# Performance work log

Hardware: AMD Instinct MI355X
Metric: run time of the kernel (lower is better)

## Reference

```python
import jax, jax.numpy as jnp
import numpy as np

B, D, H, F, L, M, MEM, ACT, STO, HID = 2048, 1024, 8, 4096, 2, 256, 16, 32, 1024, 1024
HD = D // H
SCALE = HD ** -0.5
EPS = 1e-4


def rmsnorm(x, w):
    return x * jax.lax.rsqrt(jnp.mean(x * x, axis=-1, keepdims=True) + EPS) * w


def setup_inputs() -> dict:
    key = jax.random.key(0)
    ks = iter(jax.random.split(key, 32))

    def nrm(shape, scale=0.02):
        return jax.random.normal(next(ks), shape, dtype=jnp.float32) * scale

    return {
        'stoch': jax.random.normal(next(ks), (B, STO), dtype=jnp.float32),
        'deter': jax.random.normal(next(ks), (B, D), dtype=jnp.float32),
        'action': jax.random.normal(next(ks), (B, ACT), dtype=jnp.float32),
        'memory': jax.random.normal(next(ks), (B, MEM, D), dtype=jnp.float32),
        'inp_w1': nrm((STO + ACT, HID)), 'inp_b1': jnp.zeros((HID,), jnp.float32),
        'inp_nw': jnp.ones((HID,), jnp.float32),
        'inp_w2': nrm((HID, D)), 'inp_b2': jnp.zeros((D,), jnp.float32),
        'Wq': nrm((L, D, D)), 'bq': jnp.zeros((L, D), jnp.float32),
        'Wk': nrm((L, D, D)), 'bk': jnp.zeros((L, D), jnp.float32),
        'Wv': nrm((L, D, D)), 'bv': jnp.zeros((L, D), jnp.float32),
        'Wo': nrm((L, D, D)), 'bo': jnp.zeros((L, D), jnp.float32),
        'rel_emb': nrm((L, 2 * M + 1, H)),
        'n1w': jnp.ones((L, D), jnp.float32), 'n2w': jnp.ones((L, D), jnp.float32),
        'ffw1': nrm((L, D, F)), 'ffb1': jnp.zeros((L, F), jnp.float32),
        'ffw2': nrm((L, F, D)), 'ffb2': jnp.zeros((L, D), jnp.float32),
        'fnw': jnp.ones((D,), jnp.float32),
    }


def reference(stoch, deter, action, memory, inp_w1, inp_b1, inp_nw, inp_w2, inp_b2,
              Wq, bq, Wk, bk, Wv, bv, Wo, bo, rel_emb, n1w, n2w,
              ffw1, ffb1, ffw2, ffb2, fnw):
    # action normalization: denominator is detached in torch
    a = action / jax.lax.stop_gradient(jnp.maximum(jnp.abs(action), 1.0))
    tok = jnp.concatenate([stoch.reshape(stoch.shape[0], -1), a], axis=-1)
    tok = jax.nn.silu(rmsnorm(tok @ inp_w1 + inp_b1, inp_nw)) @ inp_w2 + inp_b2  # [B,D]
    seq = jnp.concatenate([memory, tok[:, None, :]], axis=1)  # [B,S,D], S = MEM+1
    S = seq.shape[1]
    rel = jnp.clip(jnp.arange(S)[:, None] - jnp.arange(S)[None, :], -M, M) + M  # [S,S]
    for l in range(L):
        xn = rmsnorm(seq, n1w[l])
        q = (xn @ Wq[l] + bq[l]).reshape(-1, S, H, HD)
        k = (xn @ Wk[l] + bk[l]).reshape(-1, S, H, HD)
        v = (xn @ Wv[l] + bv[l]).reshape(-1, S, H, HD)
        bias = rel_emb[l][rel].transpose(2, 0, 1)  # [H,S,S]
        scores = jnp.einsum('bqhd,bkhd->bhqk', q, k) * SCALE + bias[None]
        probs = jax.nn.softmax(scores, axis=-1)
        att = jnp.einsum('bhqk,bkhd->bqhd', probs, v).reshape(-1, S, D)
        seq = seq + (att @ Wo[l] + bo[l])
        xn2 = rmsnorm(seq, n2w[l])
        seq = seq + (jax.nn.gelu(xn2 @ ffw1[l] + ffb1[l], approximate=False) @ ffw2[l] + ffb2[l])
    new_deter = rmsnorm(seq[:, -1] + deter, fnw)
    new_mem = jax.lax.stop_gradient(seq[:, -MEM:])
    return (new_deter, new_mem)
```

## Files before the change

### kernel.cpp

```cpp
#include <hip/hip_runtime.h>
#include <hip/hip_bf16.h>
#include <math.h>

#define NB 2048
#define ND 1024
#define NH 8
#define NHD 128
#define NF 4096
#define NL 2
#define NMEM 16
#define NS 17
#define NROWS (NB*NS)
#define NTOK 1056
#define SCALE_ATT 0.08838834764831845f

typedef unsigned short u16;
typedef unsigned int u32;

typedef __bf16 bf16x8 __attribute__((ext_vector_type(8)));
typedef float f32x4 __attribute__((ext_vector_type(4)));

__device__ __forceinline__ float bf2f(u16 h) {
  union { u32 u; float f; } c; c.u = ((u32)h) << 16; return c.f;
}
__device__ __forceinline__ u16 f2bf(float f) {
  union { float ff; u32 u; } c; c.ff = f;
  return (u16)((c.u + 0x7FFFu + ((c.u >> 16) & 1u)) >> 16);
}
__device__ __forceinline__ bf16x8 as_b8(uint4 u) {
  union { uint4 u; bf16x8 b; } c; c.u = u; return c.b;
}

__device__ __forceinline__ void gload16(const void* g, void* l) {
  __builtin_amdgcn_global_load_lds(
      (const __attribute__((address_space(1))) void*)(uintptr_t)g,
      (__attribute__((address_space(3))) void*)(u32)(uintptr_t)l,
      16, 0, 0);
}

__device__ __forceinline__ float gelu_fast(float x) {
  float u = x * (0.7978845608f + 0.0356774081f * x * x);
  return x * (1.0f / (1.0f + __expf(-2.0f * u)));
}

__device__ __forceinline__ void pack_tile(const float* __restrict__ src,
                                          u16* __restrict__ dst,
                                          int K, int N, int n0, int k0,
                                          float* tile )
{
  int tx = threadIdx.x & 31, ty = threadIdx.x >> 5;
#pragma unroll
  for (int r = ty; r < 32; r += 8)
    tile[r * 33 + tx] = src[(size_t)(k0 + r) * N + n0 + tx];
  __syncthreads();
#pragma unroll
  for (int r = ty; r < 32; r += 8)
    dst[(size_t)(n0 + r) * K + k0 + tx] = f2bf(tile[tx * 33 + r]);
}

__global__ __launch_bounds__(256)
void pack_wT_k(const float* __restrict__ src, u16* __restrict__ dst, int K, int N)
{
  __shared__ float tile[32 * 33];
  pack_tile(src, dst, K, N, blockIdx.x * 32, blockIdx.y * 32, tile);
}

__global__ __launch_bounds__(256)
void pack_layer_k(const float* __restrict__ wq, const float* __restrict__ wk,
                  const float* __restrict__ wv, const float* __restrict__ wo,
                  const float* __restrict__ w1, const float* __restrict__ w2,
                  const float* __restrict__ bq, const float* __restrict__ bk,
                  const float* __restrict__ bv,
                  u16* __restrict__ qkvT, u16* __restrict__ oT,
                  u16* __restrict__ f1T, u16* __restrict__ f2T,
                  float* __restrict__ BQKV)
{
  __shared__ float tile[32 * 33];
  int id = blockIdx.x;
  if (id < 4096) {
    int which = id >> 10, l = id & 1023;
    const float* src = which == 0 ? wq : which == 1 ? wk : which == 2 ? wv : wo;
    u16* dst = which == 3 ? oT : qkvT + (size_t)which * 1048576;
    pack_tile(src, dst, 1024, 1024, (l & 31) * 32, (l >> 5) * 32, tile);
  } else if (id < 8192) {
    int l = id - 4096;
    pack_tile(w1, f1T, 1024, 4096, (l & 127) * 32, (l >> 7) * 32, tile);
  } else if (id < 12288) {
    int l = id - 8192;
    pack_tile(w2, f2T, 4096, 1024, (l & 31) * 32, (l >> 5) * 32, tile);
  } else {
    int j = (id - 12288) * 256 + threadIdx.x;
    if (j < 3072)
      BQKV[j] = (j < 1024) ? bq[j] : (j < 2048 ? bk[j - 1024] : bv[j - 2048]);
  }
}

template<int EPI>
__global__ __launch_bounds__(256)
void gemm2_k(const u16* __restrict__ A, int lda,
             const u16* __restrict__ BT, int ldb,
             const float* __restrict__ bias,
             u16* __restrict__ Cb, int ldc,
             int K)
{
  __shared__ __align__(16) u16 Asm[2][128 * 32];
  __shared__ __align__(16) u16 Bsm[2][128 * 32];
  const int tid  = threadIdx.x;
  const int lane = tid & 63;
  const int wv   = tid >> 6;
  const int wm   = wv >> 1, wn = wv & 1;
  const int lr   = lane & 15;
  const int kb   = lane >> 4;

  const int gx = gridDim.x;
  const int nwg = gx * gridDim.y;
  int bid = blockIdx.y * gx + blockIdx.x;
  if ((nwg & 7) == 0) bid = (bid & 7) * (nwg >> 3) + (bid >> 3);
  const int bx = bid % gx, by = bid / gx;
  const long bmBase = (long)by * 128;
  const int  bnBase = bx * 128;

  const int srow = tid >> 2;
  const int skc  = ((tid & 3) ^ ((srow >> 1) & 3)) * 8;
  const u16* aG0 = A  + (size_t)(bmBase + srow) * lda + skc;
  const u16* aG1 = aG0 + (size_t)64 * lda;
  const u16* bG0 = BT + (size_t)(bnBase + srow) * ldb + skc;
  const u16* bG1 = bG0 + (size_t)64 * ldb;
  const int wbase = (tid & ~63) * 8;
  const int rslot = (kb ^ ((lr >> 1) & 3)) * 8;

  f32x4 acc[4][4];
#pragma unroll
  for (int m = 0; m < 4; ++m)
#pragma unroll
    for (int n = 0; n < 4; ++n)
      acc[m][n] = (f32x4){0.0f, 0.0f, 0.0f, 0.0f};

  const int nk = K >> 5;
  {
    u16* aL = &Asm[0][wbase];
    u16* bL = &Bsm[0][wbase];
    gload16(aG0, aL);
    gload16(aG1, aL + 2048);
    gload16(bG0, bL);
    gload16(bG1, bL + 2048);
  }
  asm volatile("s_waitcnt vmcnt(0)" ::: "memory");
  __builtin_amdgcn_s_barrier();

  for (int i = 0; i < nk; ++i) {
    const int cur = i & 1;
    if (i + 1 < nk) {
      const int kt = (i + 1) << 5;
      u16* aL = &Asm[cur ^ 1][wbase];
      u16* bL = &Bsm[cur ^ 1][wbase];
      gload16(aG0 + kt, aL);
      gload16(aG1 + kt, aL + 2048);
      gload16(bG0 + kt, bL);
      gload16(bG1 + kt, bL + 2048);
    }
    bf16x8 af[4], bfv[4];
#pragma unroll
    for (int m = 0; m < 4; ++m)
      af[m] = as_b8(*(const uint4*)&Asm[cur][(wm * 64 + m * 16 + lr) * 32 + rslot]);
#pragma unroll
    for (int n = 0; n < 4; ++n)
      bfv[n] = as_b8(*(const uint4*)&Bsm[cur][(wn * 64 + n * 16 + lr) * 32 + rslot]);
#pragma unroll
    for (int m = 0; m < 4; ++m)
#pragma unroll
      for (int n = 0; n < 4; ++n)
        acc[m][n] = __builtin_amdgcn_mfma_f32_16x16x32_bf16(af[m], bfv[n], acc[m][n], 0, 0, 0);
    asm volatile("s_waitcnt vmcnt(0)" ::: "memory");
    __builtin_amdgcn_s_barrier();
  }

#pragma unroll
  for (int m = 0; m < 4; ++m) {
#pragma unroll
    for (int n = 0; n < 4; ++n) {
      int gcol = bnBase + wn * 64 + n * 16 + lr;
      float bv = bias[gcol];
      long growb = bmBase + wm * 64 + m * 16 + (lane >> 4) * 4;
#pragma unroll
      for (int i = 0; i < 4; ++i) {
        float val = acc[m][n][i] + bv;
        long row = growb + i;
        u16* p = Cb + (size_t)row * ldc + gcol;
        if (EPI == 1) val = gelu_fast(val);
        if (EPI == 2) val += bf2f(*p);
        *p = f2bf(val);
      }
    }
  }
}

__global__ __launch_bounds__(256)
void prep_tokcat_k(const float* __restrict__ stoch, const float* __restrict__ action,
                   u16* __restrict__ tok)
{
  size_t idx = (size_t)blockIdx.x * 256 + threadIdx.x;
  if (idx >= (size_t)NB * NTOK) return;
  int b = (int)(idx / NTOK), j = (int)(idx % NTOK);
  float v;
  if (j < 1024) {
    v = stoch[(size_t)b * 1024 + j];
  } else {
    float a = action[(size_t)b * 32 + (j - 1024)];
    v = a / fmaxf(fabsf(a), 1.0f);
  }
  tok[idx] = f2bf(v);
}

__global__ __launch_bounds__(256)
void rmsnorm_bf16_k(const u16* __restrict__ X, const float* __restrict__ w,
                    u16* __restrict__ Y)
{
  const int wv = threadIdx.x >> 6, lane = threadIdx.x & 63;
  const size_t row = (size_t)blockIdx.x * 4 + wv;
  const u16* x = X + row * 1024 + lane * 16;
  union { u16 s[16]; uint4 u[2]; } iv;
  iv.u[0] = ((const uint4*)x)[0];
  iv.u[1] = ((const uint4*)x)[1];
  float f[16];
  float ss = 0.0f;
#pragma unroll
  for (int j = 0; j < 16; ++j) { f[j] = bf2f(iv.s[j]); ss += f[j] * f[j]; }
#pragma unroll
  for (int o = 1; o < 64; o <<= 1) ss += __shfl_xor(ss, o, 64);
  const float r = rsqrtf(ss * (1.0f / 1024.0f) + 1e-4f);
  const float* wp = w + lane * 16;
  union { u16 s[16]; uint4 u[2]; } ob;
#pragma unroll
  for (int j = 0; j < 16; ++j) ob.s[j] = f2bf(f[j] * r * wp[j]);
  uint4* dst = (uint4*)(Y + row * 1024 + lane * 16);
  dst[0] = ob.u[0];
  dst[1] = ob.u[1];
}

__global__ __launch_bounds__(256)
void rmsnorm_silu_k(u16* __restrict__ X, const float* __restrict__ w)
{
  const int wv = threadIdx.x >> 6, lane = threadIdx.x & 63;
  const size_t row = (size_t)blockIdx.x * 4 + wv;
  u16* x = X + row * 1024 + lane * 16;
  union { u16 s[16]; uint4 u[2]; } iv;
  iv.u[0] = ((const uint4*)x)[0];
  iv.u[1] = ((const uint4*)x)[1];
  float f[16];
  float ss = 0.0f;
#pragma unroll
  for (int j = 0; j < 16; ++j) { f[j] = bf2f(iv.s[j]); ss += f[j] * f[j]; }
#pragma unroll
  for (int o = 1; o < 64; o <<= 1) ss += __shfl_xor(ss, o, 64);
  const float r = rsqrtf(ss * (1.0f / 1024.0f) + 1e-4f);
  const float* wp = w + lane * 16;
  union { u16 s[16]; uint4 u[2]; } ob;
#pragma unroll
  for (int j = 0; j < 16; ++j) {
    float n = f[j] * r * wp[j];
    ob.s[j] = f2bf(n / (1.0f + __expf(-n)));
  }
  ((uint4*)x)[0] = ob.u[0];
  ((uint4*)x)[1] = ob.u[1];
}

__global__ __launch_bounds__(256)
void init_seq_k(const float* __restrict__ mem, u16* __restrict__ seq)
{
  size_t idx = ((size_t)blockIdx.x * 256 + threadIdx.x) * 8;
  if (idx >= (size_t)NB * 16 * 1024) return;
  size_t b = idx / (16 * 1024), rem = idx % (16 * 1024);
  float4 v0 = *(const float4*)&mem[idx];
  float4 v1 = *(const float4*)&mem[idx + 4];
  union { u16 s[8]; uint4 u; } ob;
  ob.s[0] = f2bf(v0.x); ob.s[1] = f2bf(v0.y); ob.s[2] = f2bf(v0.z); ob.s[3] = f2bf(v0.w);
  ob.s[4] = f2bf(v1.x); ob.s[5] = f2bf(v1.y); ob.s[6] = f2bf(v1.z); ob.s[7] = f2bf(v1.w);
  *(uint4*)&seq[b * (size_t)NS * 1024 + rem] = ob.u;
}

__global__ __launch_bounds__(256)
void copy_mem_k(const u16* __restrict__ seq, float* __restrict__ out)
{
  size_t idx = ((size_t)blockIdx.x * 256 + threadIdx.x) * 8;
  if (idx >= (size_t)NB * 16 * 1024) return;
  size_t b = idx / (16 * 1024), rem = idx % (16 * 1024);
  union { u16 s[8]; uint4 u; } iv;
  iv.u = *(const uint4*)&seq[b * (size_t)NS * 1024 + 1024 + rem];
  float4 o0, o1;
  o0.x = bf2f(iv.s[0]); o0.y = bf2f(iv.s[1]); o0.z = bf2f(iv.s[2]); o0.w = bf2f(iv.s[3]);
  o1.x = bf2f(iv.s[4]); o1.y = bf2f(iv.s[5]); o1.z = bf2f(iv.s[6]); o1.w = bf2f(iv.s[7]);
  *(float4*)&out[idx] = o0;
  *(float4*)&out[idx + 4] = o1;
}

__global__ __launch_bounds__(256)
void final_deter_k(const u16* __restrict__ seq, const float* __restrict__ deter,
                   const float* __restrict__ fnw, float* __restrict__ out)
{
  int b = blockIdx.x;
  const u16* xs = seq + ((size_t)b * NS + 16) * 1024;
  const float* dt = deter + (size_t)b * 1024;
  int t = threadIdx.x;
  union { u16 s[4]; uint2 u; } iv;
  iv.u = *(const uint2*)&xs[t * 4];
  float v[4];
#pragma unroll
  for (int j = 0; j < 4; ++j) v[j] = bf2f(iv.s[j]) + dt[t * 4 + j];
  float ss = v[0] * v[0] + v[1] * v[1] + v[2] * v[2] + v[3] * v[3];
#pragma unroll
  for (int o = 1; o < 64; o <<= 1) ss += __shfl_xor(ss, o, 64);
  __shared__ float red[4];
  if ((t & 63) == 0) red[t >> 6] = ss;
  __syncthreads();
  float tot = red[0] + red[1] + red[2] + red[3];
  float r = rsqrtf(tot * (1.0f / 1024.0f) + 1e-4f);
  float4 ov;
  ov.x = v[0] * r * fnw[t * 4 + 0];
  ov.y = v[1] * r * fnw[t * 4 + 1];
  ov.z = v[2] * r * fnw[t * 4 + 2];
  ov.w = v[3] * r * fnw[t * 4 + 3];
  *(float4*)&out[(size_t)b * 1024 + t * 4] = ov;
}

#define LSTR 132
__global__ __launch_bounds__(256)
void attn_k(const u16* __restrict__ QKV, const float* __restrict__ rel,
            u16* __restrict__ O)
{
  __shared__ float qs[NS * LSTR];
  __shared__ float ks[NS * LSTR];
  __shared__ float vs[NS * LSTR];
  __shared__ float sc[NS * 20];
  int bh = blockIdx.x;
  int b = bh >> 3, h = bh & 7;
  int t = threadIdx.x;
  const size_t rowb = (size_t)b * NS * 3072 + h * 128;
  for (int e = t; e < NS * 16; e += 256) {
    int i = e >> 4, d = (e & 15) * 8;
    size_t off = rowb + (size_t)i * 3072 + d;
    uint4 q4 = *(const uint4*)(QKV + off);
    uint4 k4 = *(const uint4*)(QKV + off + 1024);
    uint4 v4 = *(const uint4*)(QKV + off + 2048);
    const u16* qp = (const u16*)&q4;
    const u16* kp = (const u16*)&k4;
    const u16* vp = (const u16*)&v4;
#pragma unroll
    for (int j = 0; j < 8; ++j) {
      qs[i * LSTR + d + j] = bf2f(qp[j]);
      ks[i * LSTR + d + j] = bf2f(kp[j]);
      vs[i * LSTR + d + j] = bf2f(vp[j]);
    }
  }
  __syncthreads();
  for (int e = t; e < NS * NS; e += 256) {
    int i = e / NS, j = e % NS;
    const float4* q4 = (const float4*)&qs[i * LSTR];
    const float4* k4 = (const float4*)&ks[j * LSTR];
    float s = 0.0f;
#pragma unroll
    for (int dd = 0; dd < 32; ++dd) {
      float4 a = q4[dd], bb = k4[dd];
      s += a.x * bb.x + a.y * bb.y + a.z * bb.z + a.w * bb.w;
    }
    sc[i * 20 + j] = s * SCALE_ATT + rel[(i - j + 256) * 8 + h];
  }
  __syncthreads();
  if (t < NS) {
    float mx = -1e30f;
    for (int j = 0; j < NS; ++j) mx = fmaxf(mx, sc[t * 20 + j]);
    float sum = 0.0f;
    for (int j = 0; j < NS; ++j) { float e = __expf(sc[t * 20 + j] - mx); sc[t * 20 + j] = e; sum += e; }
    float inv = 1.0f / sum;
    for (int j = 0; j < NS; ++j) sc[t * 20 + j] *= inv;
  }
  __syncthreads();
  const size_t obase = (size_t)b * NS * 1024 + h * 128;
  for (int e = t; e < NS * 128; e += 256) {
    int i = e >> 7, d = e & 127;
    float o = 0.0f;
#pragma unroll
    for (int j = 0; j < NS; ++j) o += sc[i * 20 + j] * vs[j * LSTR + d];
    O[obase + (size_t)i * 1024 + d] = f2bf(o);
  }
}

extern "C" void kernel_launch(void* const* d_in, const int* in_sizes, int n_in,
                              void* d_out, int out_size, void* d_ws, size_t ws_size,
                              hipStream_t stream)
{
  const float* stoch  = (const float*)d_in[0];
  const float* deter  = (const float*)d_in[1];
  const float* action = (const float*)d_in[2];
  const float* memory = (const float*)d_in[3];
  const float* inp_w1 = (const float*)d_in[4];
  const float* inp_b1 = (const float*)d_in[5];
  const float* inp_nw = (const float*)d_in[6];
  const float* inp_w2 = (const float*)d_in[7];
  const float* inp_b2 = (const float*)d_in[8];
  const float* Wq = (const float*)d_in[9];
  const float* bq = (const float*)d_in[10];
  const float* Wk = (const float*)d_in[11];
  const float* bk = (const float*)d_in[12];
  const float* Wv = (const float*)d_in[13];
  const float* bv = (const float*)d_in[14];
  const float* Wo = (const float*)d_in[15];
  const float* bo = (const float*)d_in[16];
  const float* rel_emb = (const float*)d_in[17];
  const float* n1w = (const float*)d_in[18];
  const float* n2w = (const float*)d_in[19];
  const float* ffw1 = (const float*)d_in[20];
  const float* ffb1 = (const float*)d_in[21];
  const float* ffw2 = (const float*)d_in[22];
  const float* ffb2 = (const float*)d_in[23];
  const float* fnw  = (const float*)d_in[24];
  float* out = (float*)d_out;

  char* ws = (char*)d_ws;
  u16* SEQ = (u16*)ws;
  u16* XN  = (u16*)(ws + 71303168ULL);
  u16* QKV = (u16*)(ws + 142606336ULL);
  u16* FFH = QKV;
  u16* TOK = (u16*)(ws + 356515840ULL);
  u16* H1  = (u16*)(ws + 360841216ULL);
  u16* PK  = (u16*)(ws + 365035520ULL);
  float* BQKV = (float*)(ws + 390201344ULL);
  if (ws_size < 390213632ULL) return;

  dim3 blk(256);

  u16* w1T = PK;
  u16* w2T = PK + 1024 * 1056;
  pack_wT_k<<<dim3(1024 / 32, 1056 / 32), blk, 0, stream>>>(inp_w1, w1T, NTOK, 1024);
  pack_wT_k<<<dim3(1024 / 32, 1024 / 32), blk, 0, stream>>>(inp_w2, w2T, 1024, 1024);
  prep_tokcat_k<<<(NB * NTOK + 255) / 256, blk, 0, stream>>>(stoch, action, TOK);
  gemm2_k<0><<<dim3(8, 16), blk, 0, stream>>>(TOK, NTOK, w1T, NTOK, inp_b1, H1, 1024, NTOK);
  rmsnorm_silu_k<<<NB / 4, blk, 0, stream>>>(H1, inp_nw);
  gemm2_k<0><<<dim3(8, 16), blk, 0, stream>>>(H1, 1024, w2T, 1024, inp_b2, SEQ + 16 * 1024, NS * 1024, 1024);
  init_seq_k<<<(NB * 16 * 1024 / 8 + 255) / 256, blk, 0, stream>>>(memory, SEQ);

  u16* qkvT = PK;
  u16* oT  = PK + 3145728;
  u16* f1T = PK + 4194304;
  u16* f2T = PK + 8388608;

  for (int l = 0; l < NL; ++l) {
    const float* wq = Wq + (size_t)l * ND * ND;
    const float* wk = Wk + (size_t)l * ND * ND;
    const float* wv = Wv + (size_t)l * ND * ND;
    const float* wo = Wo + (size_t)l * ND * ND;
    const float* w1 = ffw1 + (size_t)l * ND * NF;
    const float* w2 = ffw2 + (size_t)l * NF * ND;
    const float* rl = rel_emb + (size_t)l * 513 * NH;

    pack_layer_k<<<12300, blk, 0, stream>>>(wq, wk, wv, wo, w1, w2,
                                            bq + l * ND, bk + l * ND, bv + l * ND,
                                            qkvT, oT, f1T, f2T, BQKV);

    rmsnorm_bf16_k<<<NROWS / 4, blk, 0, stream>>>(SEQ, n1w + l * ND, XN);
    gemm2_k<0><<<dim3(24, 272), blk, 0, stream>>>(XN, 1024, qkvT, 1024, BQKV, QKV, 3072, 1024);
    attn_k<<<NB * NH, blk, 0, stream>>>(QKV, rl, XN);
    gemm2_k<2><<<dim3(8, 272), blk, 0, stream>>>(XN, 1024, oT, 1024, bo + l * ND, SEQ, 1024, 1024);
    rmsnorm_bf16_k<<<NROWS / 4, blk, 0, stream>>>(SEQ, n2w + l * ND, XN);
    for (int c = 0; c < 2; ++c) {
      size_t r0 = (size_t)c * 17408;
      gemm2_k<1><<<dim3(32, 136), blk, 0, stream>>>(XN + r0 * 1024, 1024, f1T, 1024, ffb1 + l * NF, FFH, 4096, 1024);
      gemm2_k<2><<<dim3(8, 136), blk, 0, stream>>>(FFH, 4096, f2T, 4096, ffb2 + l * ND, SEQ + r0 * 1024, 1024, 4096);
    }
  }

  final_deter_k<<<NB, blk, 0, stream>>>(SEQ, deter, fnw, out);
  copy_mem_k<<<(NB * 16 * 1024 / 8 + 255) / 256, blk, 0, stream>>>(SEQ, out + (size_t)NB * ND);
}
```

Baseline: 3.107 ms.

## Use 2-wave GEMM blocks with 128x64 per-wave tiles and unchunked FFN

The GEMM kernel moves from 4 waves with 64x64 tiles each to 2 waves per 128x128 block, each computing a 128x64 tile with 32 accumulators. Each wave now reads A fragments in two halves, so per-wave MFMA work grows relative to LDS traffic, and each thread issues 8 global loads instead of 4. The workspace is enlarged so the FFN hidden buffer holds all rows, which removes the two-chunk loop and halves the FFN GEMM launches. The cost is much higher register pressure (128 accumulator floats per thread) and fewer waves per block for latency hiding, which may reduce occupancy.

```diff
diff --git a/kernel.cpp b/kernel.cpp
--- a/kernel.cpp
+++ b/kernel.cpp
@@ -96,7 +96,7 @@
 }
 
 template<int EPI>
-__global__ __launch_bounds__(256)
+__global__ __launch_bounds__(128)
 void gemm2_k(const u16* __restrict__ A, int lda,
              const u16* __restrict__ BT, int ldb,
              const float* __restrict__ bias,
@@ -107,8 +107,7 @@
   __shared__ __align__(16) u16 Bsm[2][128 * 32];
   const int tid  = threadIdx.x;
   const int lane = tid & 63;
-  const int wv   = tid >> 6;
-  const int wm   = wv >> 1, wn = wv & 1;
+  const int wn   = tid >> 6;
   const int lr   = lane & 15;
   const int kb   = lane >> 4;
 
@@ -122,28 +121,27 @@
 
   const int srow = tid >> 2;
   const int skc  = ((tid & 3) ^ ((srow >> 1) & 3)) * 8;
-  const u16* aG0 = A  + (size_t)(bmBase + srow) * lda + skc;
-  const u16* aG1 = aG0 + (size_t)64 * lda;
-  const u16* bG0 = BT + (size_t)(bnBase + srow) * ldb + skc;
-  const u16* bG1 = bG0 + (size_t)64 * ldb;
-  const int wbase = (tid & ~63) * 8;
+  const u16* aG = A  + (size_t)(bmBase + srow) * lda + skc;
+  const u16* bG = BT + (size_t)(bnBase + srow) * ldb + skc;
+  const int dloc = tid * 8;
   const int rslot = (kb ^ ((lr >> 1) & 3)) * 8;
 
-  f32x4 acc[4][4];
-#pragma unroll
-  for (int m = 0; m < 4; ++m)
+  f32x4 acc[8][4];
+#pragma unroll
+  for (int m = 0; m < 8; ++m)
 #pragma unroll
     for (int n = 0; n < 4; ++n)
       acc[m][n] = (f32x4){0.0f, 0.0f, 0.0f, 0.0f};
 
   const int nk = K >> 5;
   {
-    u16* aL = &Asm[0][wbase];
-    u16* bL = &Bsm[0][wbase];
-    gload16(aG0, aL);
-    gload16(aG1, aL + 2048);
-    gload16(bG0, bL);
-    gload16(bG1, bL + 2048);
+    u16* aL = &Asm[0][dloc];
+    u16* bL = &Bsm[0][dloc];
+#pragma unroll
+    for (int j = 0; j < 4; ++j) {
+      gload16(aG + (size_t)(j * 32) * lda, aL + j * 1024);
+      gload16(bG + (size_t)(j * 32) * ldb, bL + j * 1024);
+    }
   }
   asm volatile("s_waitcnt vmcnt(0)" ::: "memory");
   __builtin_amdgcn_s_barrier();
@@ -152,36 +150,45 @@
     const int cur = i & 1;
     if (i + 1 < nk) {
       const int kt = (i + 1) << 5;
-      u16* aL = &Asm[cur ^ 1][wbase];
-      u16* bL = &Bsm[cur ^ 1][wbase];
-      gload16(aG0 + kt, aL);
-      gload16(aG1 + kt, aL + 2048);
-      gload16(bG0 + kt, bL);
-      gload16(bG1 + kt, bL + 2048);
+      u16* aL = &Asm[cur ^ 1][dloc];
+      u16* bL = &Bsm[cur ^ 1][dloc];
+#pragma unroll
+      for (int j = 0; j < 4; ++j) {
+        gload16(aG + kt + (size_t)(j * 32) * lda, aL + j * 1024);
+        gload16(bG + kt + (size_t)(j * 32) * ldb, bL + j * 1024);
+      }
     }
-    bf16x8 af[4], bfv[4];
-#pragma unroll
-    for (int m = 0; m < 4; ++m)
-      af[m] = as_b8(*(const uint4*)&Asm[cur][(wm * 64 + m * 16 + lr) * 32 + rslot]);
+    bf16x8 bfv[4], af[4];
 #pragma unroll
     for (int n = 0; n < 4; ++n)
       bfv[n] = as_b8(*(const uint4*)&Bsm[cur][(wn * 64 + n * 16 + lr) * 32 + rslot]);
 #pragma unroll
     for (int m = 0; m < 4; ++m)
+      af[m] = as_b8(*(const uint4*)&Asm[cur][(m * 16 + lr) * 32 + rslot]);
+#pragma unroll
+    for (int m = 0; m < 4; ++m)
 #pragma unroll
       for (int n = 0; n < 4; ++n)
         acc[m][n] = __builtin_amdgcn_mfma_f32_16x16x32_bf16(af[m], bfv[n], acc[m][n], 0, 0, 0);
+#pragma unroll
+    for (int m = 0; m < 4; ++m)
+      af[m] = as_b8(*(const uint4*)&Asm[cur][((m + 4) * 16 + lr) * 32 + rslot]);
+#pragma unroll
+    for (int m = 0; m < 4; ++m)
+#pragma unroll
+      for (int n = 0; n < 4; ++n)
+        acc[m + 4][n] = __builtin_amdgcn_mfma_f32_16x16x32_bf16(af[m], bfv[n], acc[m + 4][n], 0, 0, 0);
     asm volatile("s_waitcnt vmcnt(0)" ::: "memory");
     __builtin_amdgcn_s_barrier();
   }
 
 #pragma unroll
-  for (int m = 0; m < 4; ++m) {
+  for (int m = 0; m < 8; ++m) {
 #pragma unroll
     for (int n = 0; n < 4; ++n) {
       int gcol = bnBase + wn * 64 + n * 16 + lr;
       float bv = bias[gcol];
-      long growb = bmBase + wm * 64 + m * 16 + (lane >> 4) * 4;
+      long growb = bmBase + m * 16 + (lane >> 4) * 4;
 #pragma unroll
       for (int i = 0; i < 4; ++i) {
         float val = acc[m][n][i] + bv;
@@ -421,22 +428,23 @@
   u16* XN  = (u16*)(ws + 71303168ULL);
   u16* QKV = (u16*)(ws + 142606336ULL);
   u16* FFH = QKV;
-  u16* TOK = (u16*)(ws + 356515840ULL);
-  u16* H1  = (u16*)(ws + 360841216ULL);
-  u16* PK  = (u16*)(ws + 365035520ULL);
-  float* BQKV = (float*)(ws + 390201344ULL);
-  if (ws_size < 390213632ULL) return;
+  u16* TOK = (u16*)(ws + 427819008ULL);
+  u16* H1  = (u16*)(ws + 432144384ULL);
+  u16* PK  = (u16*)(ws + 436338688ULL);
+  float* BQKV = (float*)(ws + 461504512ULL);
+  if (ws_size < 461516800ULL) return;
 
   dim3 blk(256);
+  dim3 blkG(128);
 
   u16* w1T = PK;
   u16* w2T = PK + 1024 * 1056;
   pack_wT_k<<<dim3(1024 / 32, 1056 / 32), blk, 0, stream>>>(inp_w1, w1T, NTOK, 1024);
   pack_wT_k<<<dim3(1024 / 32, 1024 / 32), blk, 0, stream>>>(inp_w2, w2T, 1024, 1024);
   prep_tokcat_k<<<(NB * NTOK + 255) / 256, blk, 0, stream>>>(stoch, action, TOK);
-  gemm2_k<0><<<dim3(8, 16), blk, 0, stream>>>(TOK, NTOK, w1T, NTOK, inp_b1, H1, 1024, NTOK);
+  gemm2_k<0><<<dim3(8, 16), blkG, 0, stream>>>(TOK, NTOK, w1T, NTOK, inp_b1, H1, 1024, NTOK);
   rmsnorm_silu_k<<<NB / 4, blk, 0, stream>>>(H1, inp_nw);
-  gemm2_k<0><<<dim3(8, 16), blk, 0, stream>>>(H1, 1024, w2T, 1024, inp_b2, SEQ + 16 * 1024, NS * 1024, 1024);
+  gemm2_k<0><<<dim3(8, 16), blkG, 0, stream>>>(H1, 1024, w2T, 1024, inp_b2, SEQ + 16 * 1024, NS * 1024, 1024);
   init_seq_k<<<(NB * 16 * 1024 / 8 + 255) / 256, blk, 0, stream>>>(memory, SEQ);
 
   u16* qkvT = PK;
@@ -458,15 +466,12 @@
                                             qkvT, oT, f1T, f2T, BQKV);
 
     rmsnorm_bf16_k<<<NROWS / 4, blk, 0, stream>>>(SEQ, n1w + l * ND, XN);
-    gemm2_k<0><<<dim3(24, 272), blk, 0, stream>>>(XN, 1024, qkvT, 1024, BQKV, QKV, 3072, 1024);
+    gemm2_k<0><<<dim3(24, 272), blkG, 0, stream>>>(XN, 1024, qkvT, 1024, BQKV, QKV, 3072, 1024);
     attn_k<<<NB * NH, blk, 0, stream>>>(QKV, rl, XN);
-    gemm2_k<2><<<dim3(8, 272), blk, 0, stream>>>(XN, 1024, oT, 1024, bo + l * ND, SEQ, 1024, 1024);
+    gemm2_k<2><<<dim3(8, 272), blkG, 0, stream>>>(XN, 1024, oT, 1024, bo + l * ND, SEQ, 1024, 1024);
     rmsnorm_bf16_k<<<NROWS / 4, blk, 0, stream>>>(SEQ, n2w + l * ND, XN);
-    for (int c = 0; c < 2; ++c) {
-      size_t r0 = (size_t)c * 17408;
-      gemm2_k<1><<<dim3(32, 136), blk, 0, stream>>>(XN + r0 * 1024, 1024, f1T, 1024, ffb1 + l * NF, FFH, 4096, 1024);
-      gemm2_k<2><<<dim3(8, 136), blk, 0, stream>>>(FFH, 4096, f2T, 4096, ffb2 + l * ND, SEQ + r0 * 1024, 1024, 4096);
-    }
+    gemm2_k<1><<<dim3(32, 272), blkG, 0, stream>>>(XN, 1024, f1T, 1024, ffb1 + l * NF, FFH, 4096, 1024);
+    gemm2_k<2><<<dim3(8, 272), blkG, 0, stream>>>(FFH, 4096, f2T, 4096, ffb2 + l * ND, SEQ, 1024, 4096);
   }
 
   final_deter_k<<<NB, blk, 0, stream>>>(SEQ, deter, fnw, out);
```

Result: slower. 4.402 ms (+41.7%).
